# Kernel tuning notes

Measured on AMD Instinct MI355X. Metric: run time of the kernel, lower is better.

The kernel has to match this reference:

```python
import jax, jax.numpy as jnp
import numpy as np

HIDDEN = 2048
N_HEADS = 32
N_KV = 8
HEAD_DIM = 64
B, S = 2, 2048
EPS = 1e-6
ROT_BASE = 10000.0


def _rms_norm(x, w):
    var = jnp.mean(x * x, axis=-1, keepdims=True)
    return x * jax.lax.rsqrt(var + EPS) * w


def _rotate_half(x):
    h = x.shape[-1] // 2
    return jnp.concatenate([-x[..., h:], x[..., :h]], axis=-1)


def _apply_rope(x, cos, sin):
    # x: [B,S,H,D], cos/sin: [S,D] -> broadcast over batch and heads
    c = cos[None, :, None, :]
    s = sin[None, :, None, :]
    return x * c + _rotate_half(x) * s


def setup_inputs() -> dict:
    key = jax.random.key(0)
    ks = jax.random.split(key, 12)
    sd = 0.02
    hidden_states = jax.random.normal(ks[0], (B, S, HIDDEN), dtype=jnp.float32)
    Wq = jax.random.normal(ks[1], (HIDDEN, N_HEADS * HEAD_DIM), dtype=jnp.float32) * sd
    bq = jnp.zeros((N_HEADS * HEAD_DIM,), dtype=jnp.float32)
    Wk = jax.random.normal(ks[2], (HIDDEN, N_KV * HEAD_DIM), dtype=jnp.float32) * sd
    bk = jnp.zeros((N_KV * HEAD_DIM,), dtype=jnp.float32)
    Wv = jax.random.normal(ks[3], (HIDDEN, N_KV * HEAD_DIM), dtype=jnp.float32) * sd
    bv = jnp.zeros((N_KV * HEAD_DIM,), dtype=jnp.float32)
    Wo = jax.random.normal(ks[4], (N_HEADS * HEAD_DIM, HIDDEN), dtype=jnp.float32) * sd
    bo = jnp.zeros((HIDDEN,), dtype=jnp.float32)
    qn_w = jnp.ones((HEAD_DIM,), dtype=jnp.float32)
    kn_w = jnp.ones((HEAD_DIM,), dtype=jnp.float32)
    # rotary tables (Llama convention: duplicated half-dim freqs)
    inv_freq = 1.0 / (ROT_BASE ** (np.arange(0, HEAD_DIM, 2, dtype=np.float32) / HEAD_DIM))
    t = np.arange(S, dtype=np.float32)
    freqs = np.outer(t, inv_freq)              # [S, D/2]
    emb = np.concatenate([freqs, freqs], axis=-1)  # [S, D]
    cos = jnp.asarray(np.cos(emb), dtype=jnp.float32)
    sin = jnp.asarray(np.sin(emb), dtype=jnp.float32)
    cu_seqlens = jnp.asarray([0, S, 2 * S], dtype=jnp.int32)
    return {"hidden_states": hidden_states, "Wq": Wq, "bq": bq, "Wk": Wk, "bk": bk,
            "Wv": Wv, "bv": bv, "Wo": Wo, "bo": bo, "qn_w": qn_w, "kn_w": kn_w,
            "cos": cos, "sin": sin, "cu_seqlens": cu_seqlens, "max_s": S}


def reference(hidden_states, Wq, bq, Wk, bk, Wv, bv, Wo, bo, qn_w, kn_w, cos, sin, cu_seqlens, max_s):
    b, s, _ = hidden_states.shape
    q = (hidden_states @ Wq + bq).reshape(b, s, N_HEADS, HEAD_DIM)
    k = (hidden_states @ Wk + bk).reshape(b, s, N_KV, HEAD_DIM)
    v = (hidden_states @ Wv + bv).reshape(b, s, N_KV, HEAD_DIM)
    q = _rms_norm(q, qn_w)
    k = _rms_norm(k, kn_w)
    q = _apply_rope(q, cos, sin)
    k = _apply_rope(k, cos, sin)
    # GQA: repeat_interleave kv heads to match query heads
    n_rep = N_HEADS // N_KV
    k = jnp.repeat(k, n_rep, axis=2)
    v = jnp.repeat(v, n_rep, axis=2)
    q = q.transpose(0, 2, 1, 3)  # [B,H,S,D]
    k = k.transpose(0, 2, 1, 3)
    v = v.transpose(0, 2, 1, 3)
    scale = 1.0 / jnp.sqrt(jnp.asarray(HEAD_DIM, dtype=q.dtype))
    scores = jnp.einsum("bhqd,bhkd->bhqk", q, k) * scale
    neg = jnp.finfo(scores.dtype).min
    causal = jnp.triu(jnp.ones((s, s), dtype=scores.dtype), k=1)  # [S,S]
    scores = scores + causal[None, None] * neg
    attn = jax.nn.softmax(scores, axis=-1)
    out = jnp.einsum("bhqk,bhkd->bhqd", attn, v)
    out = out.transpose(0, 2, 1, 3).reshape(b, s, N_HEADS * HEAD_DIM)
    return out @ Wo + bo
```

## Files before the change

### kernel.cpp

```cpp
#include <hip/hip_runtime.h>

typedef unsigned short u16;
typedef __attribute__((ext_vector_type(4))) float f32x4;
typedef __attribute__((ext_vector_type(16))) float f32x16;
typedef __attribute__((ext_vector_type(8))) short s16x8;
typedef __attribute__((ext_vector_type(8))) unsigned short u16x8;
typedef __attribute__((ext_vector_type(4))) unsigned short u16x4;

__device__ __forceinline__ float bf2f(u16 u) {
    union { unsigned int i; float f; } x; x.i = ((unsigned int)u) << 16; return x.f;
}
__device__ __forceinline__ u16 f2bf(float f) {
    union { float f; unsigned int i; } x; x.f = f;
    unsigned int r = x.i + 0x7FFFu + ((x.i >> 16) & 1u);
    return (u16)(r >> 16);
}
__device__ __forceinline__ void gload16(const void* g, void* l) {
    __builtin_amdgcn_global_load_lds((const __attribute__((address_space(1))) void*)g,
                                     (__attribute__((address_space(3))) void*)l, 16, 0, 0);
}
__device__ __forceinline__ unsigned cvtpk(float lo, float hi) {
    unsigned r;
    asm("v_cvt_pk_bf16_f32 %0, %1, %2" : "=v"(r) : "v"(lo), "v"(hi));
    return r;
}

#define BATCH 2
#define SEQ 2048
#define HID 2048
#define NH 32
#define NKV 8
#define HD 64
#define TOK (BATCH * SEQ)
#define NQKV 3072
#define QSCALE 0.18033688011112042f

__global__ void k_f32_to_bf16(const float* __restrict__ src, u16* __restrict__ dst, int n4) {
    int i = blockIdx.x * blockDim.x + threadIdx.x;
    if (i >= n4) return;
    f32x4 v = ((const f32x4*)src)[i];
    u16x4 o;
    o[0] = f2bf(v[0]); o[1] = f2bf(v[1]); o[2] = f2bf(v[2]); o[3] = f2bf(v[3]);
    *(u16x4*)(dst + (size_t)i * 4) = o;
}

__global__ void k_transpose_bf16(const float* __restrict__ src, u16* __restrict__ dst, int K, int N) {
    __shared__ float tile[32][33];
    int n0 = blockIdx.x * 32, k0 = blockIdx.y * 32;
    int tx = threadIdx.x, ty = threadIdx.y;
#pragma unroll
    for (int i = 0; i < 4; i++)
        tile[ty + i * 8][tx] = src[(size_t)(k0 + ty + i * 8) * N + n0 + tx];
    __syncthreads();
#pragma unroll
    for (int i = 0; i < 4; i++) {
        int n = n0 + ty + i * 8;
        dst[(size_t)n * K + k0 + tx] = f2bf(tile[tx][ty + i * 8]);
    }
}

__global__ void k_transpose_v(const u16* __restrict__ src, u16* __restrict__ dst) {
    __shared__ u16 tile[32][34];
    const u16* s = src + (size_t)blockIdx.z * SEQ * HD;
    u16* d = dst + (size_t)blockIdx.z * SEQ * HD;
    int d0 = blockIdx.x * 32;
    int s0 = blockIdx.y * 32;
    int tx = threadIdx.x, ty = threadIdx.y;
#pragma unroll
    for (int i = 0; i < 4; i++)
        tile[ty + i * 8][tx] = s[(size_t)(s0 + ty + i * 8) * HD + d0 + tx];
    __syncthreads();
#pragma unroll
    for (int i = 0; i < 4; i++)
        d[(size_t)(d0 + ty + i * 8) * SEQ + s0 + tx] = tile[tx][ty + i * 8];
}

__global__ void k_concat_bias(const float* __restrict__ bq, const float* __restrict__ bk,
                              const float* __restrict__ bv, float* __restrict__ out) {
    int i = blockIdx.x * blockDim.x + threadIdx.x;
    if (i >= NQKV) return;
    out[i] = (i < HID) ? bq[i] : (i < HID + 512 ? bk[i - HID] : bv[i - HID - 512]);
}

template <int OUT_BF16>
__global__ __launch_bounds__(256) void k_gemm_bt(const u16* __restrict__ A, const u16* __restrict__ BT,
                                                 const float* __restrict__ bias, void* __restrict__ Cout,
                                                 int M, int N, int K, int lda, int ldb) {
    __shared__ u16 As[128 * 32];
    __shared__ u16 Bs[128 * 32];
    const int t = threadIdx.x;
    const int gx = gridDim.x;
    int bid = blockIdx.y * gx + blockIdx.x;
    const int cpx = (gx * gridDim.y) >> 3;
    bid = (bid & 7) * cpx + (bid >> 3);
    const int brow = (bid / gx) * 128, bcol = (bid % gx) * 128;
    const int wid = t >> 6, lane = t & 63;
    const int wr = (wid >> 1) * 64, wc = (wid & 1) * 64;
    const int lr = lane & 15;
    const int lk = (lane >> 4) * 8;

    const int srow0 = wid * 32 + (lane >> 2);
    const int scol = (lane & 3) * 8;
    const u16* Ag0 = A + (size_t)(brow + srow0) * lda + scol;
    const u16* Ag1 = A + (size_t)(brow + srow0 + 16) * lda + scol;
    const u16* Bg0 = BT + (size_t)(bcol + srow0) * ldb + scol;
    const u16* Bg1 = BT + (size_t)(bcol + srow0 + 16) * ldb + scol;
    u16* Al0 = As + (wid * 2 + 0) * 512;
    u16* Al1 = As + (wid * 2 + 1) * 512;
    u16* Bl0 = Bs + (wid * 2 + 0) * 512;
    u16* Bl1 = Bs + (wid * 2 + 1) * 512;

    f32x4 acc[4][4] = {};
    for (int k0 = 0; k0 < K; k0 += 32) {
        __syncthreads();
        gload16(Ag0 + k0, Al0);
        gload16(Ag1 + k0, Al1);
        gload16(Bg0 + k0, Bl0);
        gload16(Bg1 + k0, Bl1);
        __syncthreads();
        s16x8 af[4], bf[4];
#pragma unroll
        for (int mi = 0; mi < 4; mi++) af[mi] = *(const s16x8*)(As + (wr + mi * 16 + lr) * 32 + lk);
#pragma unroll
        for (int ni = 0; ni < 4; ni++) bf[ni] = *(const s16x8*)(Bs + (wc + ni * 16 + lr) * 32 + lk);
#pragma unroll
        for (int mi = 0; mi < 4; mi++)
#pragma unroll
            for (int ni = 0; ni < 4; ni++)
                acc[mi][ni] = __builtin_amdgcn_mfma_f32_16x16x32_bf16(af[mi], bf[ni], acc[mi][ni], 0, 0, 0);
    }

    const int drow = ((lane >> 4) << 2);
#pragma unroll
    for (int mi = 0; mi < 4; mi++) {
#pragma unroll
        for (int ni = 0; ni < 4; ni++) {
#pragma unroll
            for (int r = 0; r < 4; r++) {
                int row = brow + wr + mi * 16 + drow + r;
                int col = bcol + wc + ni * 16 + lr;
                float v = acc[mi][ni][r] + bias[col];
                if (OUT_BF16) ((u16*)Cout)[(size_t)row * N + col] = f2bf(v);
                else          ((float*)Cout)[(size_t)row * N + col] = v;
            }
        }
    }
}

template <int OUT_BF16>
__global__ __launch_bounds__(512, 1) void k_gemm256(const u16* __restrict__ A, const u16* __restrict__ BT,
                                                    const float* __restrict__ bias, void* __restrict__ Cout,
                                                    int gxn, int K, int lda, int ldb, int N) {
    __shared__ u16 LDS[2][2][256 * 64];
    const int tid = threadIdx.x;
    const int w = tid >> 6, lane = tid & 63;
    const int wm = w >> 2, wn = w & 3;
    const int lr = lane & 15, g = lane >> 4;
    const int nwg = gridDim.x;
    int bid = blockIdx.x;
    const int cpx = nwg >> 3;
    bid = (bid & 7) * cpx + (bid >> 3);
    const int brow = (bid / gxn) * 256, bcol = (bid % gxn) * 256;

    const int lrow8 = lane >> 3;
    const int gs = (lane & 7) ^ lrow8;
    const u16* Ag[4]; const u16* Bg[4];
#pragma unroll
    for (int p = 0; p < 4; p++) {
        int row = (w * 4 + p) * 8 + lrow8;
        Ag[p] = A + (size_t)(brow + row) * lda + gs * 8;
        Bg[p] = BT + (size_t)(bcol + row) * ldb + gs * 8;
    }

    f32x4 acc[8][4] = {};

#pragma unroll
    for (int p = 0; p < 4; p++) {
        gload16(Ag[p], &LDS[0][0][(w * 4 + p) * 512]);
        gload16(Bg[p], &LDS[0][1][(w * 4 + p) * 512]);
    }
    asm volatile("s_waitcnt vmcnt(0)" ::: "memory");
    __builtin_amdgcn_s_barrier();
    asm volatile("" ::: "memory");

    const int NT = K >> 6;
    int cur = 0;
    for (int tk = 0; tk < NT; tk++) {
        const u16* Al = &LDS[cur][0][0];
        const u16* Bl = &LDS[cur][1][0];
        u16* An = &LDS[cur ^ 1][0][0];
        u16* Bn = &LDS[cur ^ 1][1][0];
        const int knext = (tk + 1) << 6;
        const bool pf = (tk + 1 < NT);
        s16x8 bfr[4][2];
#pragma unroll
        for (int p = 0; p < 4; p++) {
            s16x8 af[2][2];
#pragma unroll
            for (int j = 0; j < 2; j++) {
                const char* rowp = (const char*)Al + (size_t)(wm * 128 + (2 * p + j) * 16 + lr) * 128;
#pragma unroll
                for (int kk = 0; kk < 2; kk++)
                    af[j][kk] = *(const s16x8*)(rowp + (((kk * 4 + g) ^ (lr & 7)) << 4));
            }
            if (p == 0) {
#pragma unroll
                for (int ni = 0; ni < 4; ni++) {
                    const char* rowp = (const char*)Bl + (size_t)(wn * 64 + ni * 16 + lr) * 128;
#pragma unroll
                    for (int kk = 0; kk < 2; kk++)
                        bfr[ni][kk] = *(const s16x8*)(rowp + (((kk * 4 + g) ^ (lr & 7)) << 4));
                }
            }
            if (pf) {
                gload16(Ag[p] + knext, &An[(w * 4 + p) * 512]);
                gload16(Bg[p] + knext, &Bn[(w * 4 + p) * 512]);
            }
            __builtin_amdgcn_s_barrier();
            __builtin_amdgcn_s_setprio(1);
#pragma unroll
            for (int j = 0; j < 2; j++)
#pragma unroll
                for (int ni = 0; ni < 4; ni++) {
                    acc[2 * p + j][ni] = __builtin_amdgcn_mfma_f32_16x16x32_bf16(af[j][0], bfr[ni][0], acc[2 * p + j][ni], 0, 0, 0);
                    acc[2 * p + j][ni] = __builtin_amdgcn_mfma_f32_16x16x32_bf16(af[j][1], bfr[ni][1], acc[2 * p + j][ni], 0, 0, 0);
                }
            __builtin_amdgcn_s_setprio(0);
            __builtin_amdgcn_s_barrier();
        }
        if (pf) asm volatile("s_waitcnt vmcnt(0)" ::: "memory");
        __builtin_amdgcn_s_barrier();
        asm volatile("" ::: "memory");
        cur ^= 1;
    }

#pragma unroll
    for (int mi = 0; mi < 8; mi++) {
#pragma unroll
        for (int ni = 0; ni < 4; ni++) {
#pragma unroll
            for (int r = 0; r < 4; r++) {
                int row = brow + wm * 128 + mi * 16 + g * 4 + r;
                int col = bcol + wn * 64 + ni * 16 + lr;
                float v = acc[mi][ni][r] + bias[col];
                if (OUT_BF16) ((u16*)Cout)[(size_t)row * N + col] = f2bf(v);
                else          ((float*)Cout)[(size_t)row * N + col] = v;
            }
        }
    }
}

__global__ __launch_bounds__(256) void k_norm_rope(const u16* __restrict__ QKV,
                                                   const float* __restrict__ qn_w, const float* __restrict__ kn_w,
                                                   const float* __restrict__ cosT, const float* __restrict__ sinT,
                                                   u16* __restrict__ Qp, u16* __restrict__ Kp, u16* __restrict__ Vp) {
    int token = blockIdx.x;
    int slot = blockIdx.y * 4 + (threadIdx.x >> 6);
    int d = threadIdx.x & 63;
    int b = token >> 11, s = token & 2047;
    const u16* row = QKV + (size_t)token * NQKV;
    if (slot < 40) {
        bool isq = slot < 32;
        int h = isq ? slot : slot - 32;
        float x = isq ? bf2f(row[h * HD + d]) : bf2f(row[HID + h * HD + d]);
        float ss = x * x;
#pragma unroll
        for (int o = 32; o; o >>= 1) ss += __shfl_xor(ss, o);
        float r = rsqrtf(ss * (1.0f / 64.0f) + 1e-6f);
        float xn = x * r * (isq ? qn_w[d] : kn_w[d]);
        float part = __shfl_xor(xn, 32);
        float sign = (d < 32) ? -1.f : 1.f;
        float o = xn * cosT[s * HD + d] + sign * part * sinT[s * HD + d];
        if (isq) Qp[(((size_t)(b * NH + h) * SEQ + s) * HD) + d] = f2bf(o * QSCALE);
        else     Kp[(((size_t)(b * NKV + h) * SEQ + s) * HD) + d] = f2bf(o);
    } else {
        int h = slot - 40;
        Vp[(((size_t)(b * NKV + h) * SEQ + s) * HD) + d] = row[HID + 512 + h * HD + d];
    }
}

__global__ __launch_bounds__(256) void k_attn_mfma(const u16* __restrict__ Qp, const u16* __restrict__ Kp,
                                                   const u16* __restrict__ VpT, u16* __restrict__ AO) {
    __shared__ u16 K_lds[64 * 64];
    __shared__ u16 VT_lds[64 * 64];
    __shared__ u16 P_lds[4][32][76];
    const int bid = blockIdx.x;
    const int qt = 15 - (bid >> 6);
    const int hh = bid & 63;
    const int b = hh >> 5, h = hh & 31, kvh = h >> 2;
    const int t = threadIdx.x, w = t >> 6, lane = t & 63;
    const int q5 = lane & 31, hi = lane >> 5;
    const int qwb = qt * 128 + w * 32;
    const int q_abs = qwb + q5;

    const u16* Qb = Qp + (size_t)(b * NH + h) * SEQ * HD;
    const u16* Kb = Kp + (size_t)(b * NKV + kvh) * SEQ * HD;
    const u16* Vb = VpT + (size_t)(b * NKV + kvh) * HD * SEQ;

    s16x8 qf0 = *(const s16x8*)(Qb + (size_t)q_abs * HD + 0 * 16 + hi * 8);
    s16x8 qf1 = *(const s16x8*)(Qb + (size_t)q_abs * HD + 1 * 16 + hi * 8);
    s16x8 qf2 = *(const s16x8*)(Qb + (size_t)q_abs * HD + 2 * 16 + hi * 8);
    s16x8 qf3 = *(const s16x8*)(Qb + (size_t)q_abs * HD + 3 * 16 + hi * 8);

    f32x16 O0, O1;
#pragma unroll
    for (int r = 0; r < 16; r++) { O0[r] = 0.f; O1[r] = 0.f; }
    float m = -1e30f, l = 0.f;

    const int swz = (q5 & 7) << 4;
    const int nkt = 2 * (qt + 1);
    for (int kt = 0; kt < nkt; kt++) {
        const int k0 = kt * 64;
        __syncthreads();
#pragma unroll
        for (int i = 0; i < 2; i++) {
            int c = (w * 2 + i) * 64 + lane;
            int row = c >> 3, gslot = (c & 7) ^ (row & 7);
            gload16(Kb + (size_t)(k0 + row) * HD + gslot * 8, (char*)K_lds + (size_t)(w * 2 + i) * 1024);
            gload16(Vb + (size_t)row * SEQ + k0 + gslot * 8, (char*)VT_lds + (size_t)(w * 2 + i) * 1024);
        }
        __syncthreads();
        if (k0 > qwb + 31) continue;

        f32x16 s0, s1;
#pragma unroll
        for (int r = 0; r < 16; r++) { s0[r] = 0.f; s1[r] = 0.f; }
        __builtin_amdgcn_s_setprio(1);
#pragma unroll
        for (int dblk = 0; dblk < 4; dblk++) {
            s16x8 kf0 = *(const s16x8*)((const char*)K_lds + q5 * 128 + ((dblk * 32 + hi * 16) ^ swz));
            s16x8 kf1 = *(const s16x8*)((const char*)K_lds + (32 + q5) * 128 + ((dblk * 32 + hi * 16) ^ swz));
            s16x8 qq = (dblk == 0) ? qf0 : (dblk == 1) ? qf1 : (dblk == 2) ? qf2 : qf3;
            s0 = __builtin_amdgcn_mfma_f32_32x32x16_bf16(kf0, qq, s0, 0, 0, 0);
            s1 = __builtin_amdgcn_mfma_f32_32x32x16_bf16(kf1, qq, s1, 0, 0, 0);
        }
        __builtin_amdgcn_s_setprio(0);

        if (k0 + 63 > qwb) {
            const int qrel = q_abs - k0;
#pragma unroll
            for (int r = 0; r < 16; r++) {
                int kr = (r & 3) + 8 * (r >> 2) + 4 * hi;
                if (kr > qrel) s0[r] = -1e30f;
                if (kr + 32 > qrel) s1[r] = -1e30f;
            }
        }

        float mt = -1e30f;
#pragma unroll
        for (int r = 0; r < 16; r++) { mt = fmaxf(mt, s0[r]); mt = fmaxf(mt, s1[r]); }
        mt = fmaxf(mt, __shfl_xor(mt, 32));
        if (!__all(mt <= m + 8.0f)) {
            float mn = fmaxf(m, mt);
            float f = exp2f(m - mn);
            l *= f;
#pragma unroll
            for (int r = 0; r < 16; r++) { O0[r] *= f; O1[r] *= f; }
            m = mn;
        }
        float ps = 0.f;
#pragma unroll
        for (int r = 0; r < 16; r++) {
            float p0 = exp2f(s0[r] - m);
            float p1 = exp2f(s1[r] - m);
            s0[r] = p0; s1[r] = p1;
            ps += p0 + p1;
        }
        ps += __shfl_xor(ps, 32);
        l += ps;

#pragma unroll
        for (int i = 0; i < 8; i++) {
            int key = 2 * (i & 1) + 8 * (i >> 1) + 4 * hi;
            *(unsigned*)&P_lds[w][q5][key]      = cvtpk(s0[2 * i], s0[2 * i + 1]);
            *(unsigned*)&P_lds[w][q5][key + 32] = cvtpk(s1[2 * i], s1[2 * i + 1]);
        }

        __builtin_amdgcn_s_setprio(1);
#pragma unroll
        for (int ks = 0; ks < 4; ks++) {
            s16x8 pb  = *(const s16x8*)&P_lds[w][q5][ks * 16 + hi * 8];
            s16x8 vf0 = *(const s16x8*)((const char*)VT_lds + q5 * 128 + ((ks * 32 + hi * 16) ^ swz));
            s16x8 vf1 = *(const s16x8*)((const char*)VT_lds + (32 + q5) * 128 + ((ks * 32 + hi * 16) ^ swz));
            O0 = __builtin_amdgcn_mfma_f32_32x32x16_bf16(vf0, pb, O0, 0, 0, 0);
            O1 = __builtin_amdgcn_mfma_f32_32x32x16_bf16(vf1, pb, O1, 0, 0, 0);
        }
        __builtin_amdgcn_s_setprio(0);
    }

    float inv = 1.0f / l;
    u16* orow = AO + (size_t)(b * SEQ + q_abs) * (NH * HD) + h * HD;
#pragma unroll
    for (int db = 0; db < 2; db++) {
#pragma unroll
        for (int g2 = 0; g2 < 4; g2++) {
            u16x4 wv;
#pragma unroll
            for (int i2 = 0; i2 < 4; i2++) {
                float v = (db == 0 ? O0[g2 * 4 + i2] : O1[g2 * 4 + i2]) * inv;
                wv[i2] = f2bf(v);
            }
            *(u16x4*)(orow + db * 32 + g2 * 8 + hi * 4) = wv;
        }
    }
}

extern "C" void kernel_launch(void* const* d_in, const int* in_sizes, int n_in,
                              void* d_out, int out_size, void* d_ws, size_t ws_size,
                              hipStream_t stream) {
    const float* hs   = (const float*)d_in[0];
    const float* Wq   = (const float*)d_in[1];
    const float* bq   = (const float*)d_in[2];
    const float* Wk   = (const float*)d_in[3];
    const float* bk   = (const float*)d_in[4];
    const float* Wv   = (const float*)d_in[5];
    const float* bv   = (const float*)d_in[6];
    const float* Wo   = (const float*)d_in[7];
    const float* bo   = (const float*)d_in[8];
    const float* qn_w = (const float*)d_in[9];
    const float* kn_w = (const float*)d_in[10];
    const float* cosT = (const float*)d_in[11];
    const float* sinT = (const float*)d_in[12];

    char* ws = (char*)d_ws;
    size_t off = 0;
    auto alloc = [&](size_t bytes) { char* p = ws + off; off = (off + bytes + 255) & ~(size_t)255; return p; };
    u16*   Xb    = (u16*)  alloc((size_t)TOK * HID * 2);
    u16*   WTqkv = (u16*)  alloc((size_t)NQKV * HID * 2);
    u16*   WoT   = (u16*)  alloc((size_t)HID * HID * 2);
    float* bqkv  = (float*)alloc((size_t)NQKV * 4);
    u16*   QKV   = (u16*)  alloc((size_t)TOK * NQKV * 2);
    u16*   Qp    = (u16*)  alloc((size_t)BATCH * NH * SEQ * HD * 2);
    u16*   Kp    = (u16*)  alloc((size_t)BATCH * NKV * SEQ * HD * 2);
    u16*   Vp    = (u16*)  alloc((size_t)BATCH * NKV * SEQ * HD * 2);
    u16*   VpT   = (u16*)  alloc((size_t)BATCH * NKV * SEQ * HD * 2);
    u16*   AO    = (u16*)  alloc((size_t)TOK * HID * 2);
    (void)ws_size;

    k_f32_to_bf16<<<(TOK * HID / 4 + 255) / 256, 256, 0, stream>>>(hs, Xb, TOK * HID / 4);
    dim3 tb(32, 8);
    k_transpose_bf16<<<dim3(HID / 32, HID / 32), tb, 0, stream>>>(Wq, WTqkv, HID, HID);
    k_transpose_bf16<<<dim3(512 / 32, HID / 32), tb, 0, stream>>>(Wk, WTqkv + (size_t)HID * HID, HID, 512);
    k_transpose_bf16<<<dim3(512 / 32, HID / 32), tb, 0, stream>>>(Wv, WTqkv + (size_t)(HID + 512) * HID, HID, 512);
    k_transpose_bf16<<<dim3(HID / 32, HID / 32), tb, 0, stream>>>(Wo, WoT, HID, HID);
    k_concat_bias<<<(NQKV + 255) / 256, 256, 0, stream>>>(bq, bk, bv, bqkv);
    k_gemm256<1><<<dim3((TOK / 256) * (NQKV / 256)), 512, 0, stream>>>(Xb, WTqkv, bqkv, QKV,
                                                                        NQKV / 256, HID, HID, HID, NQKV);
    k_norm_rope<<<dim3(TOK, 12), 256, 0, stream>>>(QKV, qn_w, kn_w, cosT, sinT, Qp, Kp, Vp);
    k_transpose_v<<<dim3(HD / 32, SEQ / 32, BATCH * NKV), tb, 0, stream>>>(Vp, VpT);
    k_attn_mfma<<<BATCH * NH * (SEQ / 128), 256, 0, stream>>>(Qp, Kp, VpT, AO);
    k_gemm_bt<0><<<dim3(HID / 128, TOK / 128), 256, 0, stream>>>(AO, WoT, bo, d_out, TOK, HID, HID, HID, HID);
}
```

Before: 250.1 us.

## Pair causal query tiles per block and compute softmax row sums via MFMA

Each attention block now processes two query tiles (qt and 15-qt) sequentially, which balances causal work across blocks and halves the grid to 512 blocks. The softmax denominator is accumulated by an extra MFMA against a ones vector, replacing the per-tile scalar sum and shuffle. The change also uses a max3 tree for the row max and packs 64-bit P stores to LDS. The cost is fewer blocks in flight, about 2 per CU, plus one extra MFMA per k-step and more accumulator registers.

After: 296.6 us. 1.19x slower.

```diff
diff --git a/kernel.cpp b/kernel.cpp
--- a/kernel.cpp
+++ b/kernel.cpp
@@ -23,6 +23,9 @@
     unsigned r;
     asm("v_cvt_pk_bf16_f32 %0, %1, %2" : "=v"(r) : "v"(lo), "v"(hi));
     return r;
+}
+__device__ __forceinline__ float max3f(float a, float b, float c) {
+    return fmaxf(fmaxf(a, b), c);
 }
 
 #define BATCH 2
@@ -285,122 +288,147 @@
     __shared__ u16 VT_lds[64 * 64];
     __shared__ u16 P_lds[4][32][76];
     const int bid = blockIdx.x;
-    const int qt = 15 - (bid >> 6);
+    const int pair = bid >> 6;
     const int hh = bid & 63;
     const int b = hh >> 5, h = hh & 31, kvh = h >> 2;
     const int t = threadIdx.x, w = t >> 6, lane = t & 63;
     const int q5 = lane & 31, hi = lane >> 5;
-    const int qwb = qt * 128 + w * 32;
-    const int q_abs = qwb + q5;
 
     const u16* Qb = Qp + (size_t)(b * NH + h) * SEQ * HD;
     const u16* Kb = Kp + (size_t)(b * NKV + kvh) * SEQ * HD;
     const u16* Vb = VpT + (size_t)(b * NKV + kvh) * HD * SEQ;
 
-    s16x8 qf0 = *(const s16x8*)(Qb + (size_t)q_abs * HD + 0 * 16 + hi * 8);
-    s16x8 qf1 = *(const s16x8*)(Qb + (size_t)q_abs * HD + 1 * 16 + hi * 8);
-    s16x8 qf2 = *(const s16x8*)(Qb + (size_t)q_abs * HD + 2 * 16 + hi * 8);
-    s16x8 qf3 = *(const s16x8*)(Qb + (size_t)q_abs * HD + 3 * 16 + hi * 8);
-
-    f32x16 O0, O1;
-#pragma unroll
-    for (int r = 0; r < 16; r++) { O0[r] = 0.f; O1[r] = 0.f; }
-    float m = -1e30f, l = 0.f;
-
     const int swz = (q5 & 7) << 4;
-    const int nkt = 2 * (qt + 1);
-    for (int kt = 0; kt < nkt; kt++) {
-        const int k0 = kt * 64;
-        __syncthreads();
-#pragma unroll
-        for (int i = 0; i < 2; i++) {
-            int c = (w * 2 + i) * 64 + lane;
-            int row = c >> 3, gslot = (c & 7) ^ (row & 7);
-            gload16(Kb + (size_t)(k0 + row) * HD + gslot * 8, (char*)K_lds + (size_t)(w * 2 + i) * 1024);
-            gload16(Vb + (size_t)row * SEQ + k0 + gslot * 8, (char*)VT_lds + (size_t)(w * 2 + i) * 1024);
+    union { u16 u[8]; s16x8 v; } one_;
+#pragma unroll
+    for (int j = 0; j < 8; j++) one_.u[j] = 0x3F80;
+    const s16x8 onesv = one_.v;
+
+    for (int pass = 0; pass < 2; pass++) {
+        const int qt = pass ? pair : 15 - pair;
+        const int qwb = qt * 128 + w * 32;
+        const int q_abs = qwb + q5;
+
+        s16x8 qf0 = *(const s16x8*)(Qb + (size_t)q_abs * HD + 0 * 16 + hi * 8);
+        s16x8 qf1 = *(const s16x8*)(Qb + (size_t)q_abs * HD + 1 * 16 + hi * 8);
+        s16x8 qf2 = *(const s16x8*)(Qb + (size_t)q_abs * HD + 2 * 16 + hi * 8);
+        s16x8 qf3 = *(const s16x8*)(Qb + (size_t)q_abs * HD + 3 * 16 + hi * 8);
+
+        f32x16 O0, O1, La;
+#pragma unroll
+        for (int r = 0; r < 16; r++) { O0[r] = 0.f; O1[r] = 0.f; La[r] = 0.f; }
+        float m = -1e30f;
+
+        const int nkt = 2 * (qt + 1);
+        for (int kt = 0; kt < nkt; kt++) {
+            const int k0 = kt * 64;
+            __syncthreads();
+#pragma unroll
+            for (int i = 0; i < 2; i++) {
+                int c = (w * 2 + i) * 64 + lane;
+                int row = c >> 3, gslot = (c & 7) ^ (row & 7);
+                gload16(Kb + (size_t)(k0 + row) * HD + gslot * 8, (char*)K_lds + (size_t)(w * 2 + i) * 1024);
+                gload16(Vb + (size_t)row * SEQ + k0 + gslot * 8, (char*)VT_lds + (size_t)(w * 2 + i) * 1024);
+            }
+            __syncthreads();
+            if (k0 > qwb + 31) continue;
+
+            f32x16 s0, s1;
+#pragma unroll
+            for (int r = 0; r < 16; r++) { s0[r] = 0.f; s1[r] = 0.f; }
+            __builtin_amdgcn_s_setprio(1);
+#pragma unroll
+            for (int dblk = 0; dblk < 4; dblk++) {
+                s16x8 kf0 = *(const s16x8*)((const char*)K_lds + q5 * 128 + ((dblk * 32 + hi * 16) ^ swz));
+                s16x8 kf1 = *(const s16x8*)((const char*)K_lds + (32 + q5) * 128 + ((dblk * 32 + hi * 16) ^ swz));
+                s16x8 qq = (dblk == 0) ? qf0 : (dblk == 1) ? qf1 : (dblk == 2) ? qf2 : qf3;
+                s0 = __builtin_amdgcn_mfma_f32_32x32x16_bf16(kf0, qq, s0, 0, 0, 0);
+                s1 = __builtin_amdgcn_mfma_f32_32x32x16_bf16(kf1, qq, s1, 0, 0, 0);
+            }
+            __builtin_amdgcn_s_setprio(0);
+
+            if (k0 + 63 > qwb) {
+                const int qrel = q_abs - k0;
+#pragma unroll
+                for (int r = 0; r < 16; r++) {
+                    int kr = (r & 3) + 8 * (r >> 2) + 4 * hi;
+                    if (kr > qrel) s0[r] = -1e30f;
+                    if (kr + 32 > qrel) s1[r] = -1e30f;
+                }
+            }
+
+            float cA = max3f(s0[0], s0[1], s0[2]);
+            cA = max3f(cA, s0[3], s0[4]);
+            cA = max3f(cA, s0[5], s0[6]);
+            cA = fmaxf(cA, s0[7]);
+            float cB = max3f(s0[8], s0[9], s0[10]);
+            cB = max3f(cB, s0[11], s0[12]);
+            cB = max3f(cB, s0[13], s0[14]);
+            cB = fmaxf(cB, s0[15]);
+            float cC = max3f(s1[0], s1[1], s1[2]);
+            cC = max3f(cC, s1[3], s1[4]);
+            cC = max3f(cC, s1[5], s1[6]);
+            cC = fmaxf(cC, s1[7]);
+            float cD = max3f(s1[8], s1[9], s1[10]);
+            cD = max3f(cD, s1[11], s1[12]);
+            cD = max3f(cD, s1[13], s1[14]);
+            cD = fmaxf(cD, s1[15]);
+            float mt = max3f(cA, cB, cC);
+            mt = fmaxf(mt, cD);
+            mt = fmaxf(mt, __shfl_xor(mt, 32));
+
+            if (!__all(mt <= m + 8.0f)) {
+                float mn = fmaxf(m, mt);
+                float f = exp2f(m - mn);
+#pragma unroll
+                for (int r = 0; r < 16; r++) { O0[r] *= f; O1[r] *= f; La[r] *= f; }
+                m = mn;
+            }
+#pragma unroll
+            for (int r = 0; r < 16; r++) {
+                s0[r] = exp2f(s0[r] - m);
+                s1[r] = exp2f(s1[r] - m);
+            }
+
+#pragma unroll
+            for (int j = 0; j < 4; j++) {
+                unsigned lo0 = cvtpk(s0[4 * j], s0[4 * j + 1]);
+                unsigned hi0 = cvtpk(s0[4 * j + 2], s0[4 * j + 3]);
+                *(unsigned long long*)&P_lds[w][q5][8 * j + 4 * hi] =
+                    ((unsigned long long)hi0 << 32) | lo0;
+                unsigned lo1 = cvtpk(s1[4 * j], s1[4 * j + 1]);
+                unsigned hi1 = cvtpk(s1[4 * j + 2], s1[4 * j + 3]);
+                *(unsigned long long*)&P_lds[w][q5][32 + 8 * j + 4 * hi] =
+                    ((unsigned long long)hi1 << 32) | lo1;
+            }
+
+            __builtin_amdgcn_s_setprio(1);
+#pragma unroll
+            for (int ks = 0; ks < 4; ks++) {
+                s16x8 pb  = *(const s16x8*)&P_lds[w][q5][ks * 16 + hi * 8];
+                s16x8 vf0 = *(const s16x8*)((const char*)VT_lds + q5 * 128 + ((ks * 32 + hi * 16) ^ swz));
+                s16x8 vf1 = *(const s16x8*)((const char*)VT_lds + (32 + q5) * 128 + ((ks * 32 + hi * 16) ^ swz));
+                O0 = __builtin_amdgcn_mfma_f32_32x32x16_bf16(vf0, pb, O0, 0, 0, 0);
+                O1 = __builtin_amdgcn_mfma_f32_32x32x16_bf16(vf1, pb, O1, 0, 0, 0);
+                La = __builtin_amdgcn_mfma_f32_32x32x16_bf16(onesv, pb, La, 0, 0, 0);
+            }
+            __builtin_amdgcn_s_setprio(0);
         }
-        __syncthreads();
-        if (k0 > qwb + 31) continue;
-
-        f32x16 s0, s1;
-#pragma unroll
-        for (int r = 0; r < 16; r++) { s0[r] = 0.f; s1[r] = 0.f; }
-        __builtin_amdgcn_s_setprio(1);
-#pragma unroll
-        for (int dblk = 0; dblk < 4; dblk++) {
-            s16x8 kf0 = *(const s16x8*)((const char*)K_lds + q5 * 128 + ((dblk * 32 + hi * 16) ^ swz));
-            s16x8 kf1 = *(const s16x8*)((const char*)K_lds + (32 + q5) * 128 + ((dblk * 32 + hi * 16) ^ swz));
-            s16x8 qq = (dblk == 0) ? qf0 : (dblk == 1) ? qf1 : (dblk == 2) ? qf2 : qf3;
-            s0 = __builtin_amdgcn_mfma_f32_32x32x16_bf16(kf0, qq, s0, 0, 0, 0);
-            s1 = __builtin_amdgcn_mfma_f32_32x32x16_bf16(kf1, qq, s1, 0, 0, 0);
-        }
-        __builtin_amdgcn_s_setprio(0);
-
-        if (k0 + 63 > qwb) {
-            const int qrel = q_abs - k0;
-#pragma unroll
-            for (int r = 0; r < 16; r++) {
-                int kr = (r & 3) + 8 * (r >> 2) + 4 * hi;
-                if (kr > qrel) s0[r] = -1e30f;
-                if (kr + 32 > qrel) s1[r] = -1e30f;
-            }
-        }
-
-        float mt = -1e30f;
-#pragma unroll
-        for (int r = 0; r < 16; r++) { mt = fmaxf(mt, s0[r]); mt = fmaxf(mt, s1[r]); }
-        mt = fmaxf(mt, __shfl_xor(mt, 32));
-        if (!__all(mt <= m + 8.0f)) {
-            float mn = fmaxf(m, mt);
-            float f = exp2f(m - mn);
-            l *= f;
-#pragma unroll
-            for (int r = 0; r < 16; r++) { O0[r] *= f; O1[r] *= f; }
-            m = mn;
-        }
-        float ps = 0.f;
-#pragma unroll
-        for (int r = 0; r < 16; r++) {
-            float p0 = exp2f(s0[r] - m);
-            float p1 = exp2f(s1[r] - m);
-            s0[r] = p0; s1[r] = p1;
-            ps += p0 + p1;
-        }
-        ps += __shfl_xor(ps, 32);
-        l += ps;
-
-#pragma unroll
-        for (int i = 0; i < 8; i++) {
-            int key = 2 * (i & 1) + 8 * (i >> 1) + 4 * hi;
-            *(unsigned*)&P_lds[w][q5][key]      = cvtpk(s0[2 * i], s0[2 * i + 1]);
-            *(unsigned*)&P_lds[w][q5][key + 32] = cvtpk(s1[2 * i], s1[2 * i + 1]);
-        }
-
-        __builtin_amdgcn_s_setprio(1);
-#pragma unroll
-        for (int ks = 0; ks < 4; ks++) {
-            s16x8 pb  = *(const s16x8*)&P_lds[w][q5][ks * 16 + hi * 8];
-            s16x8 vf0 = *(const s16x8*)((const char*)VT_lds + q5 * 128 + ((ks * 32 + hi * 16) ^ swz));
-            s16x8 vf1 = *(const s16x8*)((const char*)VT_lds + (32 + q5) * 128 + ((ks * 32 + hi * 16) ^ swz));
-            O0 = __builtin_amdgcn_mfma_f32_32x32x16_bf16(vf0, pb, O0, 0, 0, 0);
-            O1 = __builtin_amdgcn_mfma_f32_32x32x16_bf16(vf1, pb, O1, 0, 0, 0);
-        }
-        __builtin_amdgcn_s_setprio(0);
-    }
-
-    float inv = 1.0f / l;
-    u16* orow = AO + (size_t)(b * SEQ + q_abs) * (NH * HD) + h * HD;
-#pragma unroll
-    for (int db = 0; db < 2; db++) {
-#pragma unroll
-        for (int g2 = 0; g2 < 4; g2++) {
-            u16x4 wv;
-#pragma unroll
-            for (int i2 = 0; i2 < 4; i2++) {
-                float v = (db == 0 ? O0[g2 * 4 + i2] : O1[g2 * 4 + i2]) * inv;
-                wv[i2] = f2bf(v);
-            }
-            *(u16x4*)(orow + db * 32 + g2 * 8 + hi * 4) = wv;
+
+        float inv = 1.0f / La[0];
+        u16* orow = AO + (size_t)(b * SEQ + q_abs) * (NH * HD) + h * HD;
+#pragma unroll
+        for (int db = 0; db < 2; db++) {
+#pragma unroll
+            for (int g2 = 0; g2 < 4; g2++) {
+                u16x4 wv;
+#pragma unroll
+                for (int i2 = 0; i2 < 4; i2++) {
+                    float v = (db == 0 ? O0[g2 * 4 + i2] : O1[g2 * 4 + i2]) * inv;
+                    wv[i2] = f2bf(v);
+                }
+                *(u16x4*)(orow + db * 32 + g2 * 8 + hi * 4) = wv;
+            }
         }
     }
 }
@@ -448,6 +476,6 @@
                                                                         NQKV / 256, HID, HID, HID, NQKV);
     k_norm_rope<<<dim3(TOK, 12), 256, 0, stream>>>(QKV, qn_w, kn_w, cosT, sinT, Qp, Kp, Vp);
     k_transpose_v<<<dim3(HD / 32, SEQ / 32, BATCH * NKV), tb, 0, stream>>>(Vp, VpT);
-    k_attn_mfma<<<BATCH * NH * (SEQ / 128), 256, 0, stream>>>(Qp, Kp, VpT, AO);
+    k_attn_mfma<<<BATCH * NH * 8, 256, 0, stream>>>(Qp, Kp, VpT, AO);
     k_gemm_bt<0><<<dim3(HID / 128, TOK / 128), 256, 0, stream>>>(AO, WoT, bo, d_out, TOK, HID, HID, HID, HID);
 }
```

## Fuse RMSNorm and RoPE into QKV GEMM epilogue, drop intermediate QKV buffer

Applied to the files above, without the earlier changes.

The QKV projection GEMM now applies per-head RMS normalisation and rotary embedding in its epilogue. Each wave's 64-column slice maps to exactly one head, so the norm is reduced with lane shuffles and the results are written straight into the Q/K/V head-major buffers. This removes the separate norm/rope kernel launch and the round trip of the bf16 QKV intermediate through global memory. In exchange the epilogue does more work with scattered cos/sin loads, and Q/K are now normalised from fp32 accumulators rather than from bf16-rounded values.

Result: faster. 236.2 us (-5.6%).

```diff
diff --git a/kernel.cpp b/kernel.cpp
--- a/kernel.cpp
+++ b/kernel.cpp
@@ -147,10 +147,12 @@
     }
 }
 
-template <int OUT_BF16>
-__global__ __launch_bounds__(512, 1) void k_gemm256(const u16* __restrict__ A, const u16* __restrict__ BT,
-                                                    const float* __restrict__ bias, void* __restrict__ Cout,
-                                                    int gxn, int K, int lda, int ldb, int N) {
+__global__ __launch_bounds__(512, 1) void k_gemm256_qkv(const u16* __restrict__ A, const u16* __restrict__ BT,
+                                                        const float* __restrict__ bias,
+                                                        const float* __restrict__ qn_w, const float* __restrict__ kn_w,
+                                                        const float* __restrict__ cosT, const float* __restrict__ sinT,
+                                                        u16* __restrict__ Qp, u16* __restrict__ Kp, u16* __restrict__ Vp,
+                                                        int gxn, int K, int lda, int ldb) {
     __shared__ u16 LDS[2][2][256 * 64];
     const int tid = threadIdx.x;
     const int w = tid >> 6, lane = tid & 63;
@@ -234,48 +236,58 @@
         cur ^= 1;
     }
 
+    const int head = (bcol >> 6) + wn;
+    const float nw0 = (head < 32) ? qn_w[0 * 16 + lr] : kn_w[0 * 16 + lr];
+    const float nw1 = (head < 32) ? qn_w[1 * 16 + lr] : kn_w[1 * 16 + lr];
+    const float nw2 = (head < 32) ? qn_w[2 * 16 + lr] : kn_w[2 * 16 + lr];
+    const float nw3 = (head < 32) ? qn_w[3 * 16 + lr] : kn_w[3 * 16 + lr];
 #pragma unroll
     for (int mi = 0; mi < 8; mi++) {
 #pragma unroll
-        for (int ni = 0; ni < 4; ni++) {
-#pragma unroll
-            for (int r = 0; r < 4; r++) {
-                int row = brow + wm * 128 + mi * 16 + g * 4 + r;
-                int col = bcol + wn * 64 + ni * 16 + lr;
-                float v = acc[mi][ni][r] + bias[col];
-                if (OUT_BF16) ((u16*)Cout)[(size_t)row * N + col] = f2bf(v);
-                else          ((float*)Cout)[(size_t)row * N + col] = v;
-            }
-        }
-    }
-}
-
-__global__ __launch_bounds__(256) void k_norm_rope(const u16* __restrict__ QKV,
-                                                   const float* __restrict__ qn_w, const float* __restrict__ kn_w,
-                                                   const float* __restrict__ cosT, const float* __restrict__ sinT,
-                                                   u16* __restrict__ Qp, u16* __restrict__ Kp, u16* __restrict__ Vp) {
-    int token = blockIdx.x;
-    int slot = blockIdx.y * 4 + (threadIdx.x >> 6);
-    int d = threadIdx.x & 63;
-    int b = token >> 11, s = token & 2047;
-    const u16* row = QKV + (size_t)token * NQKV;
-    if (slot < 40) {
-        bool isq = slot < 32;
-        int h = isq ? slot : slot - 32;
-        float x = isq ? bf2f(row[h * HD + d]) : bf2f(row[HID + h * HD + d]);
-        float ss = x * x;
-#pragma unroll
-        for (int o = 32; o; o >>= 1) ss += __shfl_xor(ss, o);
-        float r = rsqrtf(ss * (1.0f / 64.0f) + 1e-6f);
-        float xn = x * r * (isq ? qn_w[d] : kn_w[d]);
-        float part = __shfl_xor(xn, 32);
-        float sign = (d < 32) ? -1.f : 1.f;
-        float o = xn * cosT[s * HD + d] + sign * part * sinT[s * HD + d];
-        if (isq) Qp[(((size_t)(b * NH + h) * SEQ + s) * HD) + d] = f2bf(o * QSCALE);
-        else     Kp[(((size_t)(b * NKV + h) * SEQ + s) * HD) + d] = f2bf(o);
-    } else {
-        int h = slot - 40;
-        Vp[(((size_t)(b * NKV + h) * SEQ + s) * HD) + d] = row[HID + 512 + h * HD + d];
+        for (int r = 0; r < 4; r++) {
+            int row = brow + wm * 128 + mi * 16 + g * 4 + r;
+            int b = row >> 11, s = row & 2047;
+            float v[4];
+#pragma unroll
+            for (int ni = 0; ni < 4; ni++)
+                v[ni] = acc[mi][ni][r] + bias[bcol + wn * 64 + ni * 16 + lr];
+            if (head < 40) {
+                float ss = v[0] * v[0] + v[1] * v[1] + v[2] * v[2] + v[3] * v[3];
+                ss += __shfl_xor(ss, 1);
+                ss += __shfl_xor(ss, 2);
+                ss += __shfl_xor(ss, 4);
+                ss += __shfl_xor(ss, 8);
+                float rin = rsqrtf(ss * (1.0f / 64.0f) + 1e-6f);
+                float xn[4];
+                xn[0] = v[0] * rin * nw0;
+                xn[1] = v[1] * rin * nw1;
+                xn[2] = v[2] * rin * nw2;
+                xn[3] = v[3] * rin * nw3;
+                const float* cr = cosT + (size_t)s * HD;
+                const float* sr = sinT + (size_t)s * HD;
+                float o[4];
+#pragma unroll
+                for (int ni = 0; ni < 4; ni++) {
+                    int d = ni * 16 + lr;
+                    float part = xn[ni ^ 2];
+                    float sign = (d < 32) ? -1.f : 1.f;
+                    o[ni] = xn[ni] * cr[d] + sign * part * sr[d];
+                }
+                if (head < 32) {
+                    u16* qrow = Qp + (((size_t)(b * NH + head) * SEQ + s) * HD);
+#pragma unroll
+                    for (int ni = 0; ni < 4; ni++) qrow[ni * 16 + lr] = f2bf(o[ni] * QSCALE);
+                } else {
+                    u16* krow = Kp + (((size_t)(b * NKV + head - 32) * SEQ + s) * HD);
+#pragma unroll
+                    for (int ni = 0; ni < 4; ni++) krow[ni * 16 + lr] = f2bf(o[ni]);
+                }
+            } else {
+                u16* vrow = Vp + (((size_t)(b * NKV + head - 40) * SEQ + s) * HD);
+#pragma unroll
+                for (int ni = 0; ni < 4; ni++) vrow[ni * 16 + lr] = f2bf(v[ni]);
+            }
+        }
     }
 }
 
@@ -429,7 +441,6 @@
     u16*   WTqkv = (u16*)  alloc((size_t)NQKV * HID * 2);
     u16*   WoT   = (u16*)  alloc((size_t)HID * HID * 2);
     float* bqkv  = (float*)alloc((size_t)NQKV * 4);
-    u16*   QKV   = (u16*)  alloc((size_t)TOK * NQKV * 2);
     u16*   Qp    = (u16*)  alloc((size_t)BATCH * NH * SEQ * HD * 2);
     u16*   Kp    = (u16*)  alloc((size_t)BATCH * NKV * SEQ * HD * 2);
     u16*   Vp    = (u16*)  alloc((size_t)BATCH * NKV * SEQ * HD * 2);
@@ -444,9 +455,8 @@
     k_transpose_bf16<<<dim3(512 / 32, HID / 32), tb, 0, stream>>>(Wv, WTqkv + (size_t)(HID + 512) * HID, HID, 512);
     k_transpose_bf16<<<dim3(HID / 32, HID / 32), tb, 0, stream>>>(Wo, WoT, HID, HID);
     k_concat_bias<<<(NQKV + 255) / 256, 256, 0, stream>>>(bq, bk, bv, bqkv);
-    k_gemm256<1><<<dim3((TOK / 256) * (NQKV / 256)), 512, 0, stream>>>(Xb, WTqkv, bqkv, QKV,
-                                                                        NQKV / 256, HID, HID, HID, NQKV);
-    k_norm_rope<<<dim3(TOK, 12), 256, 0, stream>>>(QKV, qn_w, kn_w, cosT, sinT, Qp, Kp, Vp);
+    k_gemm256_qkv<<<dim3((TOK / 256) * (NQKV / 256)), 512, 0, stream>>>(
+        Xb, WTqkv, bqkv, qn_w, kn_w, cosT, sinT, Qp, Kp, Vp, NQKV / 256, HID, HID, HID);
     k_transpose_v<<<dim3(HD / 32, SEQ / 32, BATCH * NKV), tb, 0, stream>>>(Vp, VpT);
     k_attn_mfma<<<BATCH * NH * (SEQ / 128), 256, 0, stream>>>(Qp, Kp, VpT, AO);
     k_gemm_bt<0><<<dim3(HID / 128, TOK / 128), 256, 0, stream>>>(AO, WoT, bo, d_out, TOK, HID, HID, HID, HID);
```
